# Kernel optimization log

Measured on AMD Instinct MI355X. Metric: run time of the kernel, lower is better.

Reference implementation:

```python
import jax, jax.numpy as jnp
import numpy as np

D_MODEL = 2048
D_STATE = 128
D_CONV = 4
EXPAND = 2
HEADDIM = 64
NGROUPS = 1
D_INNER = EXPAND * D_MODEL            # 4096
NHEADS = D_INNER // HEADDIM           # 64
D_XBC = D_INNER + 2 * NGROUPS * D_STATE   # 4352
D_IN_PROJ = 2 * D_INNER + 2 * NGROUPS * D_STATE + NHEADS  # 8512
BLOCK_LEN = 64


def _segsum(x):
    # x: (..., T) -> (..., T, T) with segsum[i, j] = sum_{j < k <= i} x[k], -inf above diag
    T = x.shape[-1]
    xc = jnp.cumsum(x, axis=-1)
    seg = xc[..., :, None] - xc[..., None, :]
    mask = jnp.tril(jnp.ones((T, T), dtype=bool))
    return jnp.where(mask, seg, -jnp.inf)


def _ssd_scan(X, A, B, C, block_len):
    # X: (b, L, h, p), A: (b, L, h), B/C: (b, L, h, n)
    b, L, h, p = X.shape
    c = L // block_len
    X = X.reshape(b, c, block_len, h, p)
    A = A.reshape(b, c, block_len, h).transpose(0, 3, 1, 2)  # b h c l
    B = B.reshape(b, c, block_len, h, -1)
    C = C.reshape(b, c, block_len, h, -1)
    A_cumsum = jnp.cumsum(A, axis=-1)                         # b h c l
    Lmat = jnp.exp(_segsum(A))                                # b h c l l
    Y_diag = jnp.einsum('bclhn,bcshn,bhcls,bcshp->bclhp', C, B, Lmat, X)
    decay_states = jnp.exp(A_cumsum[:, :, :, -1:] - A_cumsum)  # b h c l
    states = jnp.einsum('bclhn,bhcl,bclhp->bchpn', B, decay_states, X)
    init = jnp.zeros_like(states[:, :1])
    states = jnp.concatenate([init, states], axis=1)          # b (c+1) h p n
    A_last = jnp.pad(A_cumsum[:, :, :, -1], ((0, 0), (0, 0), (1, 0)))  # b h (c+1)
    decay_chunk = jnp.exp(_segsum(A_last))                    # b h (c+1) (c+1)
    new_states = jnp.einsum('bhzc,bchpn->bzhpn', decay_chunk, states)
    states = new_states[:, 1:]                                # b c h p n
    state_decay_out = jnp.exp(A_cumsum)                       # b h c l
    Y_off = jnp.einsum('bclhn,bchpn,bhcl->bclhp', C, states, state_decay_out)
    return (Y_diag + Y_off).reshape(b, L, h, p)


def _forward(x, in_proj_w, conv_w, conv_b, A_log, D, dt_bias, norm_w, out_proj_w):
    Bsz, L, _ = x.shape
    proj = x @ in_proj_w.T                                    # (B, L, d_in_proj)
    z = proj[:, :, :D_INNER]
    xBC = proj[:, :, D_INNER:D_INNER + D_XBC]
    dt_raw = proj[:, :, D_INNER + D_XBC:]
    # depthwise causal conv1d (torch pads both sides then truncates to L == left pad only)
    xBC_t = xBC.transpose(0, 2, 1)                            # (B, C, L)
    conv = jax.lax.conv_general_dilated(
        xBC_t, conv_w, window_strides=(1,), padding=[(D_CONV - 1, 0)],
        feature_group_count=D_XBC, dimension_numbers=('NCH', 'OIH', 'NCH'))
    conv = conv + conv_b[None, :, None]
    xBC = jax.nn.silu(conv).transpose(0, 2, 1)                # (B, L, d_xBC)
    x_ssm = xBC[:, :, :D_INNER]
    B_param = xBC[:, :, D_INNER:D_INNER + NGROUPS * D_STATE]
    C_param = xBC[:, :, D_INNER + NGROUPS * D_STATE:]
    dt = jax.nn.softplus(dt_raw + dt_bias)                    # (B, L, nheads)
    A = -jnp.exp(A_log)                                       # (nheads,)
    x_heads = x_ssm.reshape(Bsz, L, NHEADS, HEADDIM)
    hpg = NHEADS // NGROUPS
    X = x_heads * dt[..., None]
    A_disc = dt * A[None, None, :]
    B_heads = jnp.repeat(B_param.reshape(Bsz, L, NGROUPS, D_STATE), hpg, axis=2)
    C_heads = jnp.repeat(C_param.reshape(Bsz, L, NGROUPS, D_STATE), hpg, axis=2)
    pad_len = (BLOCK_LEN - L % BLOCK_LEN) % BLOCK_LEN
    if pad_len > 0:
        X = jnp.pad(X, ((0, 0), (0, pad_len), (0, 0), (0, 0)))
        A_disc = jnp.pad(A_disc, ((0, 0), (0, pad_len), (0, 0)))
        B_heads = jnp.pad(B_heads, ((0, 0), (0, pad_len), (0, 0), (0, 0)))
        C_heads = jnp.pad(C_heads, ((0, 0), (0, pad_len), (0, 0), (0, 0)))
    Y = _ssd_scan(X, A_disc, B_heads, C_heads, BLOCK_LEN)[:, :L]
    Y = Y + x_heads * D[None, None, :, None]
    y = Y.reshape(Bsz, L, D_INNER)
    y = y * jax.nn.silu(z)
    rms = jnp.sqrt(jnp.mean(y * y, axis=-1, keepdims=True) + 1e-5)
    y = y / rms * norm_w
    return y @ out_proj_w.T


def setup_inputs() -> dict:
    key = jax.random.key(0)
    ks = jax.random.split(key, 8)
    x = jax.random.normal(ks[0], (2, 2048, D_MODEL), dtype=jnp.float32)
    in_proj_w = jax.random.normal(ks[1], (D_IN_PROJ, D_MODEL), dtype=jnp.float32) * 0.02
    conv_w = jax.random.normal(ks[2], (D_XBC, 1, D_CONV), dtype=jnp.float32) * 0.2
    conv_b = jnp.zeros((D_XBC,), dtype=jnp.float32)
    A_log = jnp.log(jnp.arange(1, NHEADS + 1, dtype=jnp.float32))
    D = jnp.ones((NHEADS,), dtype=jnp.float32)
    dt_bias = jax.random.normal(ks[3], (NHEADS,), dtype=jnp.float32) * 0.1
    norm_w = jnp.ones((D_INNER,), dtype=jnp.float32)
    out_proj_w = jax.random.normal(ks[4], (D_MODEL, D_INNER), dtype=jnp.float32) * 0.02
    return {"x": x, "in_proj_w": in_proj_w, "conv_w": conv_w, "conv_b": conv_b,
            "A_log": A_log, "D": D, "dt_bias": dt_bias, "norm_w": norm_w,
            "out_proj_w": out_proj_w}


def reference(x, in_proj_w, conv_w, conv_b, A_log, D, dt_bias, norm_w, out_proj_w):
    return _forward(x, in_proj_w, conv_w, conv_b, A_log, D, dt_bias, norm_w, out_proj_w)
```

## Files before the change

### kernel.cpp

```cpp
#include <hip/hip_runtime.h>
#include <cstddef>
#include <cstdint>

#define B_SZ    2
#define SEQ     2048
#define DMODEL  2048
#define DINNER  4096
#define DSTATE  128
#define NHEADS  64
#define HEADDIM 64
#define DXBC    4352
#define NPROJ   8448
#define CHUNK   64
#define NCHUNK  32
#define TOKENS  (B_SZ*SEQ)

typedef __attribute__((ext_vector_type(8))) short short8;
typedef __attribute__((ext_vector_type(4))) float floatx4;

__device__ inline float us2f(unsigned short u) {
  union { uint32_t i; float f; } c; c.i = ((uint32_t)u) << 16; return c.f;
}
__device__ inline unsigned short f2us(float f) {
  union { float f; uint32_t i; } c; c.f = f;
  uint32_t r = (c.i + 0x7fffu + ((c.i >> 16) & 1u)) >> 16;
  return (unsigned short)r;
}
__device__ inline float plo(uint32_t v) {
  union { uint32_t i; float f; } c; c.i = v << 16; return c.f;
}
__device__ inline float phi(uint32_t v) {
  union { uint32_t i; float f; } c; c.i = v & 0xffff0000u; return c.f;
}

__global__ __launch_bounds__(256) void cast_f32_bf16(
    const float* __restrict__ src, unsigned short* __restrict__ dst, int n) {
  int i = (blockIdx.x * 256 + threadIdx.x) * 4;
  if (i < n) {
    float4 v = *(const float4*)(src + i);
    ushort4 o;
    o.x = f2us(v.x); o.y = f2us(v.y); o.z = f2us(v.z); o.w = f2us(v.w);
    *(ushort4*)(dst + i) = o;
  }
}

template<int OUT_BF16>
__global__ __launch_bounds__(256) void gemm_bt_mfma(
    const unsigned short* __restrict__ A, const unsigned short* __restrict__ B,
    void* __restrict__ Cout, int M, int N, int K) {
  __shared__ unsigned short sA[128*32];
  __shared__ unsigned short sB[128*32];
  const int tid  = threadIdx.x;
  const int lane = tid & 63;
  const int wave = tid >> 6;
  const int bm = blockIdx.y * 128;
  const int bn = blockIdx.x * 128;
  const int wm = (wave >> 1) * 64;
  const int wn = (wave & 1) * 64;
  const int fr = lane & 15;
  const int fq = lane >> 4;

  floatx4 acc[4][4];
  #pragma unroll
  for (int i = 0; i < 4; ++i)
    #pragma unroll
    for (int j = 0; j < 4; ++j) acc[i][j] = (floatx4){0.f, 0.f, 0.f, 0.f};

  const int g0 = tid * 8;
  for (int k0 = 0; k0 < K; k0 += 32) {
    __syncthreads();
    #pragma unroll
    for (int r = 0; r < 2; ++r) {
      int g = r * 2048 + g0;
      int row = g >> 5, col = g & 31;
      const unsigned short* gp = A + (size_t)(bm + row) * K + k0 + col;
      __builtin_amdgcn_global_load_lds(
          (const __attribute__((address_space(1))) uint32_t*)gp,
          (__attribute__((address_space(3))) uint32_t*)(sA + g), 16, 0, 0);
    }
    #pragma unroll
    for (int r = 0; r < 2; ++r) {
      int g = r * 2048 + g0;
      int row = g >> 5, col = g & 31;
      const unsigned short* gp = B + (size_t)(bn + row) * K + k0 + col;
      __builtin_amdgcn_global_load_lds(
          (const __attribute__((address_space(1))) uint32_t*)gp,
          (__attribute__((address_space(3))) uint32_t*)(sB + g), 16, 0, 0);
    }
    __syncthreads();

    short8 af[4], bfr[4];
    #pragma unroll
    for (int i = 0; i < 4; ++i)
      af[i] = *(const short8*)(sA + (wm + i*16 + fr) * 32 + fq * 8);
    #pragma unroll
    for (int j = 0; j < 4; ++j)
      bfr[j] = *(const short8*)(sB + (wn + j*16 + fr) * 32 + fq * 8);
    #pragma unroll
    for (int i = 0; i < 4; ++i)
      #pragma unroll
      for (int j = 0; j < 4; ++j)
        acc[i][j] = __builtin_amdgcn_mfma_f32_16x16x32_bf16(af[i], bfr[j], acc[i][j], 0, 0, 0);
  }

  #pragma unroll
  for (int i = 0; i < 4; ++i) {
    #pragma unroll
    for (int j = 0; j < 4; ++j) {
      int col = bn + wn + j*16 + fr;
      #pragma unroll
      for (int r = 0; r < 4; ++r) {
        int row = bm + wm + i*16 + fq*4 + r;
        if (OUT_BF16)
          ((unsigned short*)Cout)[(size_t)row * N + col] = f2us(acc[i][j][r]);
        else
          ((float*)Cout)[(size_t)row * N + col] = acc[i][j][r];
      }
    }
  }
}

__device__ inline void loadA4(const float* p, float* d) {
  float4 v = *(const float4*)p; d[0]=v.x; d[1]=v.y; d[2]=v.z; d[3]=v.w;
}
__device__ inline void loadA4(const unsigned short* p, float* d) {
  ushort4 v = *(const ushort4*)p;
  d[0]=us2f(v.x); d[1]=us2f(v.y); d[2]=us2f(v.z); d[3]=us2f(v.w);
}
__device__ inline void store8(float* C, size_t off, const float* v) {
  *(float4*)(C + off)     = make_float4(v[0], v[1], v[2], v[3]);
  *(float4*)(C + off + 4) = make_float4(v[4], v[5], v[6], v[7]);
}
__device__ inline void store8(unsigned short* C, size_t off, const float* v) {
  ushort4 a; a.x=f2us(v[0]); a.y=f2us(v[1]); a.z=f2us(v[2]); a.w=f2us(v[3]);
  ushort4 b; b.x=f2us(v[4]); b.y=f2us(v[5]); b.z=f2us(v[6]); b.w=f2us(v[7]);
  *(ushort4*)(C + off) = a; *(ushort4*)(C + off + 4) = b;
}

template<typename AT, typename OT>
__global__ __launch_bounds__(256) void gemm_nt(
    const AT* __restrict__ A, const float* __restrict__ Bw,
    OT* __restrict__ C, int M, int N, int K) {
  __shared__ float As[16][128+4];
  __shared__ float Bs[16][128+4];
  const int bm = blockIdx.y * 128;
  const int bn = blockIdx.x * 128;
  const int tid = threadIdx.x;
  const int tx = tid & 15, ty = tid >> 4;

  float acc[8][8];
  #pragma unroll
  for (int i = 0; i < 8; ++i)
    #pragma unroll
    for (int j = 0; j < 8; ++j) acc[i][j] = 0.f;

  for (int k0 = 0; k0 < K; k0 += 16) {
    #pragma unroll
    for (int r = 0; r < 2; ++r) {
      int i = tid + r * 256;
      int m  = i >> 2;
      int kv = (i & 3) << 2;
      float va[4];
      loadA4(A + (size_t)(bm + m) * K + k0 + kv, va);
      As[kv+0][m] = va[0]; As[kv+1][m] = va[1]; As[kv+2][m] = va[2]; As[kv+3][m] = va[3];
      float vb[4] = {0.f, 0.f, 0.f, 0.f};
      if (bn + m < N) loadA4(Bw + (size_t)(bn + m) * K + k0 + kv, vb);
      Bs[kv+0][m] = vb[0]; Bs[kv+1][m] = vb[1]; Bs[kv+2][m] = vb[2]; Bs[kv+3][m] = vb[3];
    }
    __syncthreads();
    #pragma unroll
    for (int kk = 0; kk < 16; ++kk) {
      float ra[8], rb[8];
      *(float4*)&ra[0] = *(const float4*)&As[kk][ty*8];
      *(float4*)&ra[4] = *(const float4*)&As[kk][ty*8+4];
      *(float4*)&rb[0] = *(const float4*)&Bs[kk][tx*8];
      *(float4*)&rb[4] = *(const float4*)&Bs[kk][tx*8+4];
      #pragma unroll
      for (int i = 0; i < 8; ++i)
        #pragma unroll
        for (int j = 0; j < 8; ++j) acc[i][j] += ra[i] * rb[j];
    }
    __syncthreads();
  }
  #pragma unroll
  for (int i = 0; i < 8; ++i) {
    int m  = bm + ty*8 + i;
    int n0 = bn + tx*8;
    if (n0 < N) store8(C, (size_t)m * N + n0, &acc[i][0]);
  }
}

__global__ __launch_bounds__(256) void dt_gemm(
    const float* __restrict__ x, const float* __restrict__ W,
    float* __restrict__ dtr) {
  __shared__ float sX[32][64];
  __shared__ float sW[32][64];
  const int tid = threadIdx.x;
  const int t0 = blockIdx.x * 64;
  const int tx = tid & 15;
  const int ty = tid >> 4;
  const float* Wdt = W + (size_t)NPROJ * DMODEL;

  float acc[4][4];
  #pragma unroll
  for (int i = 0; i < 4; ++i)
    #pragma unroll
    for (int j = 0; j < 4; ++j) acc[i][j] = 0.f;

  const int r  = tid >> 3;
  const int kq = (tid & 7) * 4;

  for (int k0 = 0; k0 < DMODEL; k0 += 32) {
    __syncthreads();
    #pragma unroll
    for (int rr = 0; rr < 2; ++rr) {
      int t = r + rr * 32;
      float4 v = *(const float4*)(x + (size_t)(t0 + t) * DMODEL + k0 + kq);
      sX[kq+0][t] = v.x; sX[kq+1][t] = v.y; sX[kq+2][t] = v.z; sX[kq+3][t] = v.w;
    }
    #pragma unroll
    for (int rr = 0; rr < 2; ++rr) {
      int hh = r + rr * 32;
      float4 v = *(const float4*)(Wdt + (size_t)hh * DMODEL + k0 + kq);
      sW[kq+0][hh] = v.x; sW[kq+1][hh] = v.y; sW[kq+2][hh] = v.z; sW[kq+3][hh] = v.w;
    }
    __syncthreads();
    #pragma unroll
    for (int kk = 0; kk < 32; ++kk) {
      float4 ra = *(const float4*)&sX[kk][ty*4];
      float4 rb = *(const float4*)&sW[kk][tx*4];
      float a[4] = {ra.x, ra.y, ra.z, ra.w};
      float b[4] = {rb.x, rb.y, rb.z, rb.w};
      #pragma unroll
      for (int i = 0; i < 4; ++i)
        #pragma unroll
        for (int j = 0; j < 4; ++j)
          acc[i][j] += a[i] * b[j];
    }
  }
  #pragma unroll
  for (int i = 0; i < 4; ++i) {
    float4 o = make_float4(acc[i][0], acc[i][1], acc[i][2], acc[i][3]);
    *(float4*)(dtr + (size_t)(t0 + ty*4 + i) * NHEADS + tx*4) = o;
  }
}

__global__ __launch_bounds__(256) void bc_conv_g(
    const unsigned short* __restrict__ proj, const float* __restrict__ cw,
    const float* __restrict__ cb, unsigned short* __restrict__ bcact,
    float* __restrict__ gbuf) {
  const int c = blockIdx.x & 31;
  const int b = blockIdx.x >> 5;
  const int tid = threadIdx.x;
  const int t0 = b * SEQ + c * CHUNK;
  __shared__ unsigned short sB[64*130];
  __shared__ unsigned short sC[64*130];
  for (int i = tid; i < 64*256; i += 256) {
    int s = i >> 8, ch = i & 255;
    int cx = 4096 + ch;
    int lb = c * CHUNK + s;
    float acc = cb[cx];
    #pragma unroll
    for (int j = 0; j < 4; ++j) {
      int ll = lb - 3 + j;
      if (ll >= 0)
        acc += cw[cx*4 + j] * us2f(proj[(size_t)(b*SEQ + ll) * NPROJ + DINNER + cx]);
    }
    float v = acc / (1.f + expf(-acc));
    unsigned short uv = f2us(v);
    if (ch < 128) sB[s*130 + ch] = uv;
    else          sC[s*130 + (ch - 128)] = uv;
    bcact[(size_t)(t0 + s) * 256 + ch] = uv;
  }
  __syncthreads();
  const int l = tid >> 2, q = tid & 3;
  float g[16];
  #pragma unroll
  for (int j = 0; j < 16; ++j) g[j] = 0.f;
  const uint32_t* Cu = (const uint32_t*)&sC[l * 130];
  for (int u = 0; u < 64; ++u) {
    uint32_t cv = Cu[u];
    float c0 = plo(cv), c1 = phi(cv);
    #pragma unroll
    for (int j = 0; j < 16; ++j) {
      uint32_t bv = ((const uint32_t*)&sB[(q*16 + j) * 130])[u];
      g[j] += c0 * plo(bv) + c1 * phi(bv);
    }
  }
  float* gr = gbuf + ((size_t)(b*NCHUNK + c)) * 4096 + l*64 + q*16;
  #pragma unroll
  for (int j = 0; j < 16; ++j) gr[j] = g[j];
}

__global__ __launch_bounds__(256, 4) void ssd_phase_a2_mfma(
    const unsigned short* __restrict__ proj, const unsigned short* __restrict__ bcact,
    const float* __restrict__ dtr, const float* __restrict__ cw,
    const float* __restrict__ cb, const float* __restrict__ A_log,
    const float* __restrict__ dt_bias, const float* __restrict__ gbuf,
    const float* __restrict__ Dv,
    unsigned short* __restrict__ cs, float* __restrict__ acs,
    unsigned short* __restrict__ yscan) {
  const int h = blockIdx.x & 63;
  const int c = (blockIdx.x >> 6) & 31;
  const int b = blockIdx.x >> 11;
  const int tid = threadIdx.x;
  const int t0 = b * SEQ + c * CHUNK;
  const int lane = tid & 63, wave = tid >> 6;
  const int fr = lane & 15, fq = lane >> 4;

  __shared__ __align__(16) unsigned short sBt[128*72];
  __shared__ __align__(16) unsigned short sXh[64*72];
  __shared__ __align__(16) unsigned short sW[64*72];
  __shared__ float sdt[64], sAc[64], sdecay[64];

  const float Ah = -expf(A_log[h]);
  if (tid < 64) {
    float raw = dtr[(size_t)(t0 + tid) * NHEADS + h] + dt_bias[h];
    float dt = (raw > 20.f) ? raw : log1pf(expf(raw));
    sdt[tid] = dt;
    float v = dt * Ah;
    #pragma unroll
    for (int off = 1; off < 64; off <<= 1) {
      float o = __shfl_up(v, off, 64);
      if (tid >= off) v += o;
    }
    sAc[tid] = v;
    float alast = __shfl(v, 63, 64);
    sdecay[tid] = expf(alast - v);
    acs[((size_t)((b*NHEADS + h)*NCHUNK + c))*64 + tid] = v;
  }
  __syncthreads();
  for (int i = tid; i < 64*128; i += 256) {
    int s = i >> 7, n = i & 127;
    float v = us2f(bcact[(size_t)(t0 + s) * 256 + n]) * sdt[s] * sdecay[s];
    sBt[n*72 + s] = f2us(v);
  }
  for (int i = tid; i < 64*64; i += 256) {
    int s = i >> 6, p = i & 63;
    int cx = h * HEADDIM + p;
    int lb = c * CHUNK + s;
    float acc = cb[cx];
    #pragma unroll
    for (int j = 0; j < 4; ++j) {
      int ll = lb - 3 + j;
      if (ll >= 0)
        acc += cw[cx*4 + j] * us2f(proj[(size_t)(b*SEQ + ll) * NPROJ + DINNER + cx]);
    }
    float xh = acc / (1.f + expf(-acc));
    sXh[p*72 + s] = f2us(xh);
  }
  {
    const float* gr = gbuf + ((size_t)(b*NCHUNK + c)) * 4096;
    for (int i = tid; i < 4096; i += 256) {
      int l = i >> 6, s = i & 63;
      float w = (s <= l) ? gr[i] * expf(sAc[l] - sAc[s]) * sdt[s] : 0.f;
      sW[l*72 + s] = f2us(w);
    }
  }
  __syncthreads();

  floatx4 accy[4];
  #pragma unroll
  for (int j = 0; j < 4; ++j) accy[j] = (floatx4){0.f, 0.f, 0.f, 0.f};
  #pragma unroll
  for (int k0 = 0; k0 < 64; k0 += 32) {
    short8 af = *(const short8*)(sW + (wave*16 + fr)*72 + k0 + fq*8);
    #pragma unroll
    for (int j = 0; j < 4; ++j) {
      short8 bf = *(const short8*)(sXh + (j*16 + fr)*72 + k0 + fq*8);
      accy[j] = __builtin_amdgcn_mfma_f32_16x16x32_bf16(af, bf, accy[j], 0, 0, 0);
    }
  }
  const float Dh = Dv[h];
  #pragma unroll
  for (int j = 0; j < 4; ++j) {
    int p = j*16 + fr;
    #pragma unroll
    for (int r = 0; r < 4; ++r) {
      int l = wave*16 + fq*4 + r;
      float yd = accy[j][r] + us2f(sXh[p*72 + l]) * Dh;
      yscan[(size_t)(t0 + l) * DINNER + h*HEADDIM + p] = f2us(yd);
    }
  }
  floatx4 accs[8];
  #pragma unroll
  for (int j = 0; j < 8; ++j) accs[j] = (floatx4){0.f, 0.f, 0.f, 0.f};
  #pragma unroll
  for (int k0 = 0; k0 < 64; k0 += 32) {
    short8 af = *(const short8*)(sXh + (wave*16 + fr)*72 + k0 + fq*8);
    #pragma unroll
    for (int j = 0; j < 8; ++j) {
      short8 bf = *(const short8*)(sBt + (j*16 + fr)*72 + k0 + fq*8);
      accs[j] = __builtin_amdgcn_mfma_f32_16x16x32_bf16(af, bf, accs[j], 0, 0, 0);
    }
  }
  const size_t csb = ((size_t)((b*NHEADS + h)*NCHUNK + c)) * (HEADDIM*DSTATE);
  #pragma unroll
  for (int j = 0; j < 8; ++j) {
    int n = j*16 + fr;
    #pragma unroll
    for (int r = 0; r < 4; ++r) {
      int p = wave*16 + fq*4 + r;
      cs[csb + p*128 + n] = f2us(accs[j][r]);
    }
  }
}

__global__ __launch_bounds__(256) void ssd_scan_states(
    unsigned short* __restrict__ cs, const float* __restrict__ acs) {
  int idx = blockIdx.x * 256 + threadIdx.x;
  int e  = idx & 8191;
  int bh = idx >> 13;
  float S = 0.f;
  for (int c = 0; c < NCHUNK; ++c) {
    float al = acs[((size_t)bh*NCHUNK + c)*64 + 63];
    size_t o = ((size_t)bh*NCHUNK + c)*(HEADDIM*DSTATE) + e;
    S = S * expf(al) + us2f(cs[o]);
    cs[o] = f2us(S);
  }
}

__global__ __launch_bounds__(256, 4) void ssd_phase_c_mfma(
    const unsigned short* __restrict__ bcact, const unsigned short* __restrict__ cs,
    const float* __restrict__ acs, unsigned short* __restrict__ yscan) {
  const int h = blockIdx.x & 63;
  const int c = (blockIdx.x >> 6) & 31;
  const int b = blockIdx.x >> 11;
  const int tid = threadIdx.x;
  const int t0 = b * SEQ + c * CHUNK;
  const int lane = tid & 63, wave = tid >> 6;
  const int fr = lane & 15, fq = lane >> 4;

  __shared__ __align__(16) unsigned short sC[64*136];
  __shared__ __align__(16) unsigned short sS[64*136];
  __shared__ float seAc[64];

  const size_t csb = ((size_t)((b*NHEADS + h)*NCHUNK + c)) * (HEADDIM*DSTATE);
  for (int i = tid; i < 8192; i += 256) {
    int p = i >> 7, n = i & 127;
    sS[p*136 + n] = cs[csb + i];
  }
  for (int i = tid; i < 8192; i += 256) {
    int l = i >> 7, n = i & 127;
    sC[l*136 + n] = bcact[(size_t)(t0 + l) * 256 + 128 + n];
  }
  if (tid < 64) seAc[tid] = expf(acs[((size_t)((b*NHEADS + h)*NCHUNK + c))*64 + tid]);
  __syncthreads();

  floatx4 acc[4];
  #pragma unroll
  for (int j = 0; j < 4; ++j) acc[j] = (floatx4){0.f, 0.f, 0.f, 0.f};
  #pragma unroll
  for (int k0 = 0; k0 < 128; k0 += 32) {
    short8 af = *(const short8*)(sC + (wave*16 + fr)*136 + k0 + fq*8);
    #pragma unroll
    for (int j = 0; j < 4; ++j) {
      short8 bf = *(const short8*)(sS + (j*16 + fr)*136 + k0 + fq*8);
      acc[j] = __builtin_amdgcn_mfma_f32_16x16x32_bf16(af, bf, acc[j], 0, 0, 0);
    }
  }
  #pragma unroll
  for (int j = 0; j < 4; ++j) {
    int p = j*16 + fr;
    #pragma unroll
    for (int r = 0; r < 4; ++r) {
      int l = wave*16 + fq*4 + r;
      size_t yi = (size_t)(t0 + l) * DINNER + h*HEADDIM + p;
      yscan[yi] = f2us(us2f(yscan[yi]) + acc[j][r] * seAc[l]);
    }
  }
}

__global__ __launch_bounds__(256) void gate_rmsnorm2(
    const unsigned short* __restrict__ proj, const float* __restrict__ norm_w,
    unsigned short* __restrict__ yscan) {
  const int t = blockIdx.x;
  const int tid = threadIdx.x;
  __shared__ float ybuf[DINNER];
  __shared__ float wpart[4];
  __shared__ float sinv;
  float ss = 0.f;
  for (int i = tid; i < DINNER; i += 256) {
    float zv = us2f(proj[(size_t)t * NPROJ + i]);
    float yv = us2f(yscan[(size_t)t * DINNER + i]) * (zv / (1.f + expf(-zv)));
    ybuf[i] = yv;
    ss += yv * yv;
  }
  #pragma unroll
  for (int off = 32; off > 0; off >>= 1) ss += __shfl_down(ss, off, 64);
  if ((tid & 63) == 0) wpart[tid >> 6] = ss;
  __syncthreads();
  if (tid == 0) {
    float tot = wpart[0] + wpart[1] + wpart[2] + wpart[3];
    sinv = 1.f / sqrtf(tot / (float)DINNER + 1e-5f);
  }
  __syncthreads();
  float inv = sinv;
  for (int i = tid; i < DINNER; i += 256)
    yscan[(size_t)t * DINNER + i] = f2us(ybuf[i] * inv * norm_w[i]);
}

__global__ __launch_bounds__(512) void ssd_fused(
    const unsigned short* __restrict__ proj, const float* __restrict__ dtr,
    const float* __restrict__ cw, const float* __restrict__ cb,
    const float* __restrict__ A_log, const float* __restrict__ dt_bias,
    unsigned short* __restrict__ yscan) {
  const int h = blockIdx.x & 63;
  const int b = blockIdx.x >> 6;
  const int tid = threadIdx.x;

  __shared__ unsigned short sB[64*130];
  __shared__ unsigned short sC[64*130];
  __shared__ unsigned short sX[64*66];
  __shared__ float sW[64*65];
  __shared__ float sdt[64], sAc[64], sdecay[64], seAc[64];

  const float Ah = -expf(A_log[h]);
  const float dbias = dt_bias[h];

  float S[16];
  #pragma unroll
  for (int j = 0; j < 16; ++j) S[j] = 0.f;

  const int lG  = tid >> 3;
  const int oc  = tid & 7;

  for (int c = 0; c < NCHUNK; ++c) {
    const int t0 = b * SEQ + c * CHUNK;
    __syncthreads();
    if (tid < 64) {
      float raw = dtr[(size_t)(t0 + tid) * NHEADS + h] + dbias;
      sdt[tid] = (raw > 20.f) ? raw : log1pf(expf(raw));
    }
    for (int i = tid; i < 64*256; i += 512) {
      int s = i >> 8, ch = i & 255;
      int cx = 4096 + ch;
      int lb = c * CHUNK + s;
      float acc = cb[cx];
      #pragma unroll
      for (int j = 0; j < 4; ++j) {
        int ll = lb - 3 + j;
        if (ll >= 0)
          acc += cw[cx*4 + j] * us2f(proj[(size_t)(b*SEQ + ll) * NPROJ + DINNER + cx]);
      }
      float v = acc / (1.f + expf(-acc));
      if (ch < 128) sB[s*130 + ch] = f2us(v);
      else          sC[s*130 + (ch - 128)] = f2us(v);
    }
    __syncthreads();
    if (tid == 0) {
      float run = 0.f;
      for (int s = 0; s < CHUNK; ++s) { run += sdt[s] * Ah; sAc[s] = run; }
    }
    __syncthreads();
    if (tid < 64) {
      float last = sAc[63];
      sdecay[tid] = expf(last - sAc[tid]);
      seAc[tid]   = expf(sAc[tid]);
    }
    for (int i = tid; i < 64*64; i += 512) {
      int s = i >> 6, p = i & 63;
      int cx = h * HEADDIM + p;
      int lb = c * CHUNK + s;
      float acc = cb[cx];
      #pragma unroll
      for (int j = 0; j < 4; ++j) {
        int ll = lb - 3 + j;
        if (ll >= 0)
          acc += cw[cx*4 + j] * us2f(proj[(size_t)(b*SEQ + ll) * NPROJ + DINNER + cx]);
      }
      float v = acc / (1.f + expf(-acc));
      sX[s*66 + p] = f2us(v * sdt[s]);
    }
    __syncthreads();

    float g[8];
    #pragma unroll
    for (int j = 0; j < 8; ++j) g[j] = 0.f;
    {
      const uint32_t* Cu = (const uint32_t*)&sC[lG * 130];
      for (int u = 0; u < 64; ++u) {
        uint32_t cv = Cu[u];
        float c0 = plo(cv), c1 = phi(cv);
        #pragma unroll
        for (int j = 0; j < 8; ++j) {
          uint32_t bv = ((const uint32_t*)&sB[(oc*8 + j) * 130])[u];
          g[j] += c0 * plo(bv) + c1 * phi(bv);
        }
      }
    }
    {
      float acl = sAc[lG];
      #pragma unroll
      for (int j = 0; j < 8; ++j) {
        int s = oc*8 + j;
        sW[lG*65 + s] = (s <= lG) ? g[j] * expf(acl - sAc[s]) : 0.f;
      }
    }
    {
      float elast = expf(sAc[63]);
      #pragma unroll
      for (int j = 0; j < 16; ++j) S[j] *= elast;
      for (int s = 0; s < CHUNK; ++s) {
        float w = sdecay[s] * us2f(sX[s*66 + lG]);
        const uint32_t* Bu = (const uint32_t*)&sB[s*130 + oc*16];
        #pragma unroll
        for (int ju = 0; ju < 8; ++ju) {
          uint32_t bv = Bu[ju];
          S[2*ju]   += plo(bv) * w;
          S[2*ju+1] += phi(bv) * w;
        }
      }
    }
    __syncthreads();
    #pragma unroll
    for (int j = 0; j < 16; ++j) sB[lG*130 + oc*16 + j] = f2us(S[j]);
    __syncthreads();
    for (int o = tid; o < CHUNK*HEADDIM; o += 512) {
      int l = o >> 6, p = o & 63;
      float yd = 0.f;
      for (int s = 0; s <= l; ++s)
        yd += sW[l*65 + s] * us2f(sX[s*66 + p]);
      float yo = 0.f;
      const uint32_t* Cu = (const uint32_t*)&sC[l * 130];
      const uint32_t* Su = (const uint32_t*)&sB[p * 130];
      for (int u = 0; u < 64; ++u) {
        uint32_t cv = Cu[u], sv = Su[u];
        yo += plo(cv) * plo(sv) + phi(cv) * phi(sv);
      }
      float y = yd + yo * seAc[l];
      yscan[(size_t)(t0 + l) * DINNER + h * HEADDIM + p] = f2us(y);
    }
  }
}

__global__ __launch_bounds__(256) void gate_rmsnorm_dskip(
    const unsigned short* __restrict__ proj, const float* __restrict__ cw,
    const float* __restrict__ cb, const float* __restrict__ Dv,
    const float* __restrict__ norm_w, unsigned short* __restrict__ yscan) {
  const int t = blockIdx.x;
  const int tid = threadIdx.x;
  const int b = t >> 11, lb = t & 2047;
  __shared__ float ybuf[DINNER];
  __shared__ float wpart[4];
  __shared__ float sinv;
  float ss = 0.f;
  for (int i = tid; i < DINNER; i += 256) {
    float zv = us2f(proj[(size_t)t * NPROJ + i]);
    float acc = cb[i];
    #pragma unroll
    for (int j = 0; j < 4; ++j) {
      int ll = lb - 3 + j;
      if (ll >= 0)
        acc += cw[i*4 + j] * us2f(proj[(size_t)(b*SEQ + ll) * NPROJ + DINNER + i]);
    }
    float xh = acc / (1.f + expf(-acc));
    float yv = us2f(yscan[(size_t)t * DINNER + i]) + xh * Dv[i >> 6];
    yv = yv * (zv / (1.f + expf(-zv)));
    ybuf[i] = yv;
    ss += yv * yv;
  }
  #pragma unroll
  for (int off = 32; off > 0; off >>= 1) ss += __shfl_down(ss, off, 64);
  if ((tid & 63) == 0) wpart[tid >> 6] = ss;
  __syncthreads();
  if (tid == 0) {
    float tot = wpart[0] + wpart[1] + wpart[2] + wpart[3];
    sinv = 1.f / sqrtf(tot / (float)DINNER + 1e-5f);
  }
  __syncthreads();
  float inv = sinv;
  for (int i = tid; i < DINNER; i += 256)
    yscan[(size_t)t * DINNER + i] = f2us(ybuf[i] * inv * norm_w[i]);
}

extern "C" void kernel_launch(void* const* d_in, const int* in_sizes, int n_in,
                              void* d_out, int out_size, void* d_ws, size_t ws_size,
                              hipStream_t stream) {
  const float* x          = (const float*)d_in[0];
  const float* in_proj_w  = (const float*)d_in[1];
  const float* conv_w     = (const float*)d_in[2];
  const float* conv_b     = (const float*)d_in[3];
  const float* A_log      = (const float*)d_in[4];
  const float* Dv         = (const float*)d_in[5];
  const float* dt_bias    = (const float*)d_in[6];
  const float* norm_w     = (const float*)d_in[7];
  const float* out_proj_w = (const float*)d_in[8];
  float* out = (float*)d_out;

  unsigned short* proj  = (unsigned short*)d_ws;
  float*          dtr   = (float*)(proj + (size_t)TOKENS * NPROJ);
  unsigned short* yscan = (unsigned short*)(dtr + (size_t)TOKENS * NHEADS);
  unsigned short* cs    = yscan + (size_t)TOKENS * DINNER;
  float*          acs   = (float*)(cs + (size_t)B_SZ*NHEADS*NCHUNK*HEADDIM*DSTATE);
  unsigned short* bcact = (unsigned short*)(acs + (size_t)B_SZ*NHEADS*NCHUNK*64);
  float*          gbuf  = (float*)(bcact + (size_t)TOKENS*256);
  const size_t NEEDED = (size_t)((char*)(gbuf + (size_t)B_SZ*NCHUNK*4096) - (char*)d_ws);

  unsigned short* xb  = cs;
  unsigned short* wib = xb + (size_t)TOKENS * DMODEL;
  unsigned short* wob = proj;

  if (ws_size >= NEEDED) {
    cast_f32_bf16<<<(TOKENS*DMODEL)/1024, 256, 0, stream>>>(x, xb, TOKENS*DMODEL);
    cast_f32_bf16<<<((size_t)NPROJ*DMODEL)/1024, 256, 0, stream>>>(in_proj_w, wib, NPROJ*DMODEL);
    {
      dim3 grid(NPROJ/128, TOKENS/128);
      gemm_bt_mfma<1><<<grid, 256, 0, stream>>>(xb, wib, proj, TOKENS, NPROJ, DMODEL);
    }
    dt_gemm<<<TOKENS/64, 256, 0, stream>>>(x, in_proj_w, dtr);
    bc_conv_g<<<B_SZ*NCHUNK, 256, 0, stream>>>(proj, conv_w, conv_b, bcact, gbuf);
    ssd_phase_a2_mfma<<<B_SZ*NCHUNK*NHEADS, 256, 0, stream>>>(
        proj, bcact, dtr, conv_w, conv_b, A_log, dt_bias, gbuf, Dv, cs, acs, yscan);
    ssd_scan_states<<<(B_SZ*NHEADS*HEADDIM*DSTATE)/256, 256, 0, stream>>>(cs, acs);
    ssd_phase_c_mfma<<<B_SZ*NCHUNK*NHEADS, 256, 0, stream>>>(bcact, cs, acs, yscan);
    gate_rmsnorm2<<<TOKENS, 256, 0, stream>>>(proj, norm_w, yscan);
    cast_f32_bf16<<<((size_t)DMODEL*DINNER)/1024, 256, 0, stream>>>(out_proj_w, wob, DMODEL*DINNER);
    {
      dim3 grid(DMODEL/128, TOKENS/128);
      gemm_bt_mfma<0><<<grid, 256, 0, stream>>>(yscan, wob, out, TOKENS, DMODEL, DINNER);
    }
  } else {
    {
      dim3 grid(NPROJ/128, TOKENS/128);
      gemm_nt<float, unsigned short><<<grid, 256, 0, stream>>>(
          x, in_proj_w, proj, TOKENS, NPROJ, DMODEL);
    }
    dt_gemm<<<TOKENS/64, 256, 0, stream>>>(x, in_proj_w, dtr);
    ssd_fused<<<B_SZ*NHEADS, 512, 0, stream>>>(proj, dtr, conv_w, conv_b,
                                               A_log, dt_bias, yscan);
    gate_rmsnorm_dskip<<<TOKENS, 256, 0, stream>>>(proj, conv_w, conv_b, Dv, norm_w, yscan);
    {
      dim3 grid(DMODEL/128, TOKENS/128);
      gemm_nt<unsigned short, float><<<grid, 256, 0, stream>>>(
          yscan, out_proj_w, out, TOKENS, DMODEL, DINNER);
    }
  }
}
```

Measured before the change: 853.9 us.

## Add 256x256-tile bf16 MFMA GEMM with direct-to-LDS loads for in_proj

Introduces a new GEMM kernel for the input projection using 256x256 output tiles, 512 threads, a double-buffered LDS with XOR swizzling, and global_load_lds async copies that prefetch the next K tile while MFMAs run on the current one. The aim is more data reuse per tile and better overlap of memory with compute than the 128x128 kernel. The grid is NPROJ/256 x TOKENS/256 = 33x16 = 528 blocks at one block per CU, so wave quantization on the CU count and heavy register pressure from 32 accumulators are risks.

```diff
diff --git a/kernel.cpp b/kernel.cpp
--- a/kernel.cpp
+++ b/kernel.cpp
@@ -41,6 +41,114 @@
     ushort4 o;
     o.x = f2us(v.x); o.y = f2us(v.y); o.z = f2us(v.z); o.w = f2us(v.w);
     *(ushort4*)(dst + i) = o;
+  }
+}
+
+template<int OUT_BF16>
+__global__ __launch_bounds__(512, 1) void gemm_bt_256(
+    const unsigned short* __restrict__ A, const unsigned short* __restrict__ B,
+    void* __restrict__ Cout, int M, int N, int K) {
+  __shared__ __align__(16) unsigned short sT[2][32768];
+  const int tid  = threadIdx.x;
+  const int lane = tid & 63;
+  const int wave = tid >> 6;
+  const int wr   = wave >> 2;
+  const int wc   = wave & 3;
+  const int fr   = lane & 15;
+  const int fq   = lane >> 4;
+  const int bm   = blockIdx.y * 256;
+  const int bn   = blockIdx.x * 256;
+
+  floatx4 acc[8][4];
+  #pragma unroll
+  for (int i = 0; i < 8; ++i)
+    #pragma unroll
+    for (int j = 0; j < 4; ++j) acc[i][j] = (floatx4){0.f, 0.f, 0.f, 0.f};
+
+  const int srow = tid >> 3;
+  const int scol = 8 * ((tid & 7) ^ (srow & 7));
+  const int xorm = (fr & 7) * 8;
+
+  auto stage = [&](int c, int k0base, unsigned short* dst) {
+    const int part = c >> 2, q = c & 3;
+    const int row  = q * 64 + srow;
+    const unsigned short* g =
+        (part ? B + (size_t)(bn + row) * K : A + (size_t)(bm + row) * K) + k0base + scol;
+    unsigned short* l = dst + part * 16384 + q * 4096 + tid * 8;
+    __builtin_amdgcn_global_load_lds(
+        (const __attribute__((address_space(1))) uint32_t*)g,
+        (__attribute__((address_space(3))) uint32_t*)l, 16, 0, 0);
+  };
+
+  #pragma unroll
+  for (int c = 0; c < 8; ++c) stage(c, 0, &sT[0][0]);
+  asm volatile("s_waitcnt vmcnt(0)" ::: "memory");
+  asm volatile("s_barrier" ::: "memory");
+
+  const int NT = K >> 6;
+  for (int kt = 0; kt < NT; ++kt) {
+    const int cur = kt & 1;
+    const unsigned short* bufc = &sT[cur][0];
+    unsigned short* bufn = &sT[cur ^ 1][0];
+    const int k1 = (kt + 1) << 6;
+    const bool pre = (kt + 1 < NT);
+
+    short8 bf[2][4];
+    #pragma unroll
+    for (int p = 0; p < 4; ++p) {
+      if (p < 2 && pre) {
+        #pragma unroll
+        for (int r = 0; r < 4; ++r) stage(p * 4 + r, k1, bufn);
+      }
+      if (p == 0) {
+        #pragma unroll
+        for (int ks = 0; ks < 2; ++ks)
+          #pragma unroll
+          for (int j = 0; j < 4; ++j) {
+            int row = wc * 64 + j * 16 + fr;
+            bf[ks][j] = *(const short8*)(bufc + 16384 + row * 64 +
+                                         ((ks * 32 + fq * 8) ^ xorm));
+          }
+      }
+      short8 af[2][2];
+      #pragma unroll
+      for (int ks = 0; ks < 2; ++ks)
+        #pragma unroll
+        for (int i = 0; i < 2; ++i) {
+          int row = wr * 128 + (p * 2 + i) * 16 + fr;
+          af[ks][i] = *(const short8*)(bufc + row * 64 +
+                                       ((ks * 32 + fq * 8) ^ xorm));
+        }
+      asm volatile("s_barrier" ::: "memory");
+      __builtin_amdgcn_s_setprio(1);
+      #pragma unroll
+      for (int ks = 0; ks < 2; ++ks)
+        #pragma unroll
+        for (int i = 0; i < 2; ++i)
+          #pragma unroll
+          for (int j = 0; j < 4; ++j)
+            acc[p * 2 + i][j] = __builtin_amdgcn_mfma_f32_16x16x32_bf16(
+                af[ks][i], bf[ks][j], acc[p * 2 + i][j], 0, 0, 0);
+      __builtin_amdgcn_s_setprio(0);
+      if (p == 3) asm volatile("s_waitcnt vmcnt(0)" ::: "memory");
+      asm volatile("s_barrier" ::: "memory");
+    }
+  }
+
+  #pragma unroll
+  for (int i = 0; i < 8; ++i) {
+    #pragma unroll
+    for (int j = 0; j < 4; ++j) {
+      int col = bn + wc * 64 + j * 16 + fr;
+      #pragma unroll
+      for (int r = 0; r < 4; ++r) {
+        int row = bm + wr * 128 + i * 16 + fq * 4 + r;
+        if (OUT_BF16)
+          ((unsigned short*)Cout)[(size_t)row * N + col] = f2us(acc[i][j][r]);
+        else
+          ((float*)Cout)[(size_t)row * N + col] = acc[i][j][r];
+      }
+    }
   }
 }
 
@@ -705,8 +813,8 @@
     cast_f32_bf16<<<(TOKENS*DMODEL)/1024, 256, 0, stream>>>(x, xb, TOKENS*DMODEL);
     cast_f32_bf16<<<((size_t)NPROJ*DMODEL)/1024, 256, 0, stream>>>(in_proj_w, wib, NPROJ*DMODEL);
     {
-      dim3 grid(NPROJ/128, TOKENS/128);
-      gemm_bt_mfma<1><<<grid, 256, 0, stream>>>(xb, wib, proj, TOKENS, NPROJ, DMODEL);
+      dim3 grid(NPROJ/256, TOKENS/256);
+      gemm_bt_256<1><<<grid, 512, 0, stream>>>(xb, wib, proj, TOKENS, NPROJ, DMODEL);
     }
     dt_gemm<<<TOKENS/64, 256, 0, stream>>>(x, in_proj_w, dtr);
     bc_conv_g<<<B_SZ*NCHUNK, 256, 0, stream>>>(proj, conv_w, conv_b, bcact, gbuf);
```

Measured after the change: 849.2 us. About the same (-0.5%).

## Rewrite bf16 GEMM with triple-buffered async LDS pipeline, swizzle, and 128x256 tiles

Applied to the files above, without the earlier changes.

Replaces the single-buffered 128x128 MFMA GEMM with a 128x256 tile kernel. It prefetches two K-steps ahead into three LDS buffers using global_load_lds and partial vmcnt waits. LDS columns are XOR-swizzled to avoid bank conflicts, and workgroup ids are remapped for XCD-aware scheduling. It also raises MFMA priority and sets occupancy to 2 waves-per-EU. The intent is to hide global load latency behind MFMA work and improve reuse, at the cost of more registers (32 accumulators) and 72KB of LDS per block.

```diff
diff --git a/kernel.cpp b/kernel.cpp
--- a/kernel.cpp
+++ b/kernel.cpp
@@ -45,72 +45,97 @@
 }
 
 template<int OUT_BF16>
-__global__ __launch_bounds__(256) void gemm_bt_mfma(
+__global__ __launch_bounds__(256, 2) void gemm_bt_p3(
     const unsigned short* __restrict__ A, const unsigned short* __restrict__ B,
-    void* __restrict__ Cout, int M, int N, int K) {
-  __shared__ unsigned short sA[128*32];
-  __shared__ unsigned short sB[128*32];
+    void* __restrict__ Cout, int M, int N, int K, int GM) {
+  __shared__ __align__(16) unsigned short sT[3 * 12288];
   const int tid  = threadIdx.x;
   const int lane = tid & 63;
-  const int wave = tid >> 6;
-  const int bm = blockIdx.y * 128;
-  const int bn = blockIdx.x * 128;
-  const int wm = (wave >> 1) * 64;
-  const int wn = (wave & 1) * 64;
-  const int fr = lane & 15;
-  const int fq = lane >> 4;
-
-  floatx4 acc[4][4];
-  #pragma unroll
-  for (int i = 0; i < 4; ++i)
+  const int wc   = tid >> 6;
+  const int fr   = lane & 15;
+  const int fq   = lane >> 4;
+
+  const int nwg  = gridDim.x;
+  int wgid = blockIdx.x;
+  if ((nwg & 7) == 0) wgid = (wgid & 7) * (nwg >> 3) + (wgid >> 3);
+  const int bm = (wgid % GM) * 128;
+  const int bn = (wgid / GM) * 256;
+
+  floatx4 acc[8][4];
+  #pragma unroll
+  for (int i = 0; i < 8; ++i)
     #pragma unroll
     for (int j = 0; j < 4; ++j) acc[i][j] = (floatx4){0.f, 0.f, 0.f, 0.f};
 
-  const int g0 = tid * 8;
-  for (int k0 = 0; k0 < K; k0 += 32) {
-    __syncthreads();
-    #pragma unroll
-    for (int r = 0; r < 2; ++r) {
-      int g = r * 2048 + g0;
-      int row = g >> 5, col = g & 31;
-      const unsigned short* gp = A + (size_t)(bm + row) * K + k0 + col;
-      __builtin_amdgcn_global_load_lds(
-          (const __attribute__((address_space(1))) uint32_t*)gp,
-          (__attribute__((address_space(3))) uint32_t*)(sA + g), 16, 0, 0);
-    }
-    #pragma unroll
-    for (int r = 0; r < 2; ++r) {
-      int g = r * 2048 + g0;
-      int row = g >> 5, col = g & 31;
-      const unsigned short* gp = B + (size_t)(bn + row) * K + k0 + col;
-      __builtin_amdgcn_global_load_lds(
-          (const __attribute__((address_space(1))) uint32_t*)gp,
-          (__attribute__((address_space(3))) uint32_t*)(sB + g), 16, 0, 0);
-    }
-    __syncthreads();
-
-    short8 af[4], bfr[4];
-    #pragma unroll
-    for (int i = 0; i < 4; ++i)
-      af[i] = *(const short8*)(sA + (wm + i*16 + fr) * 32 + fq * 8);
-    #pragma unroll
-    for (int j = 0; j < 4; ++j)
-      bfr[j] = *(const short8*)(sB + (wn + j*16 + fr) * 32 + fq * 8);
-    #pragma unroll
-    for (int i = 0; i < 4; ++i)
+  auto stage = [&](int rb, int kb) {
+    unsigned short* dst = (unsigned short*)sT + rb * 12288;
+    #pragma unroll
+    for (int q = 0; q < 6; ++q) {
+      if (q < 2) {
+        int i = q * 256 + tid;
+        int row = i >> 2, slot = i & 3;
+        const unsigned short* g =
+            A + (size_t)(bm + row) * K + kb + 8 * (slot ^ ((row >> 1) & 3));
+        __builtin_amdgcn_global_load_lds(
+            (const __attribute__((address_space(1))) uint32_t*)g,
+            (__attribute__((address_space(3))) uint32_t*)(dst + i * 8), 16, 0, 0);
+      } else {
+        int i = (q - 2) * 256 + tid;
+        int row = i >> 2, slot = i & 3;
+        const unsigned short* g =
+            B + (size_t)(bn + row) * K + kb + 8 * (slot ^ ((row >> 1) & 3));
+        __builtin_amdgcn_global_load_lds(
+            (const __attribute__((address_space(1))) uint32_t*)g,
+            (__attribute__((address_space(3))) uint32_t*)(dst + 4096 + i * 8), 16, 0, 0);
+      }
+    }
+  };
+
+  const int NH = K >> 5;
+  stage(0, 0);
+  stage(1, 32);
+  asm volatile("s_waitcnt vmcnt(6)" ::: "memory");
+  asm volatile("s_barrier" ::: "memory");
+
+  int cb = 0, sb = 2;
+  for (int h = 0; h < NH; ++h) {
+    const unsigned short* buf = (const unsigned short*)sT + cb * 12288;
+    if (h + 2 < NH) stage(sb, (h + 2) << 5);
+
+    short8 af[8], bf[4];
+    #pragma unroll
+    for (int i = 0; i < 8; ++i) {
+      int row = i * 16 + fr;
+      af[i] = *(const short8*)(buf + row * 32 + 8 * (fq ^ ((row >> 1) & 3)));
+    }
+    #pragma unroll
+    for (int j = 0; j < 4; ++j) {
+      int row = wc * 64 + j * 16 + fr;
+      bf[j] = *(const short8*)(buf + 4096 + row * 32 + 8 * (fq ^ ((row >> 1) & 3)));
+    }
+    __builtin_amdgcn_s_setprio(1);
+    #pragma unroll
+    for (int i = 0; i < 8; ++i)
       #pragma unroll
       for (int j = 0; j < 4; ++j)
-        acc[i][j] = __builtin_amdgcn_mfma_f32_16x16x32_bf16(af[i], bfr[j], acc[i][j], 0, 0, 0);
-  }
-
-  #pragma unroll
-  for (int i = 0; i < 4; ++i) {
+        acc[i][j] = __builtin_amdgcn_mfma_f32_16x16x32_bf16(af[i], bf[j], acc[i][j], 0, 0, 0);
+    __builtin_amdgcn_s_setprio(0);
+
+    if (h < NH - 2) asm volatile("s_waitcnt vmcnt(6) lgkmcnt(0)" ::: "memory");
+    else            asm volatile("s_waitcnt vmcnt(0) lgkmcnt(0)" ::: "memory");
+    asm volatile("s_barrier" ::: "memory");
+    cb = (cb == 2) ? 0 : cb + 1;
+    sb = (sb == 2) ? 0 : sb + 1;
+  }
+
+  #pragma unroll
+  for (int i = 0; i < 8; ++i) {
     #pragma unroll
     for (int j = 0; j < 4; ++j) {
-      int col = bn + wn + j*16 + fr;
+      int col = bn + wc * 64 + j * 16 + fr;
       #pragma unroll
       for (int r = 0; r < 4; ++r) {
-        int row = bm + wm + i*16 + fq*4 + r;
+        int row = bm + i * 16 + fq * 4 + r;
         if (OUT_BF16)
           ((unsigned short*)Cout)[(size_t)row * N + col] = f2us(acc[i][j][r]);
         else
@@ -705,8 +730,8 @@
     cast_f32_bf16<<<(TOKENS*DMODEL)/1024, 256, 0, stream>>>(x, xb, TOKENS*DMODEL);
     cast_f32_bf16<<<((size_t)NPROJ*DMODEL)/1024, 256, 0, stream>>>(in_proj_w, wib, NPROJ*DMODEL);
     {
-      dim3 grid(NPROJ/128, TOKENS/128);
-      gemm_bt_mfma<1><<<grid, 256, 0, stream>>>(xb, wib, proj, TOKENS, NPROJ, DMODEL);
+      int nwg = (TOKENS/128) * (NPROJ/256);
+      gemm_bt_p3<1><<<nwg, 256, 0, stream>>>(xb, wib, proj, TOKENS, NPROJ, DMODEL, TOKENS/128);
     }
     dt_gemm<<<TOKENS/64, 256, 0, stream>>>(x, in_proj_w, dtr);
     bc_conv_g<<<B_SZ*NCHUNK, 256, 0, stream>>>(proj, conv_w, conv_b, bcact, gbuf);
@@ -717,8 +742,8 @@
     gate_rmsnorm2<<<TOKENS, 256, 0, stream>>>(proj, norm_w, yscan);
     cast_f32_bf16<<<((size_t)DMODEL*DINNER)/1024, 256, 0, stream>>>(out_proj_w, wob, DMODEL*DINNER);
     {
-      dim3 grid(DMODEL/128, TOKENS/128);
-      gemm_bt_mfma<0><<<grid, 256, 0, stream>>>(yscan, wob, out, TOKENS, DMODEL, DINNER);
+      int nwg = (TOKENS/128) * (DMODEL/256);
+      gemm_bt_p3<0><<<nwg, 256, 0, stream>>>(yscan, wob, out, TOKENS, DMODEL, DINNER, TOKENS/128);
     }
   } else {
     {
```

Result: faster. 796.0 us (-6.8%).
